# Kernel tuning notes

Hardware: AMD Instinct MI355X
Metric: run time of the kernel (lower is better)

Reference implementation:

```python
import jax, jax.numpy as jnp
import numpy as np


def setup_inputs() -> dict:
    key = jax.random.key(0)
    k1, k2 = jax.random.split(key)
    B, Te, Td, D = 8, 2048, 2048, 256
    encoder_outputs = jax.random.normal(k1, (B, Te, D), dtype=jnp.float32)
    decoder_outputs = jax.random.normal(k2, (B, Td, D), dtype=jnp.float32)
    return {"encoder_outputs": encoder_outputs, "decoder_outputs": decoder_outputs}


def reference(encoder_outputs, decoder_outputs):
    # score[b, e, t] = enc[b, e, :] . dec[b, t, :]   -> [B, Te, Td]
    score = jnp.einsum('bed,btd->bet', encoder_outputs, decoder_outputs)
    # softmax over the encoder-time axis (axis=1), matching K.softmax(..., axis=1)
    attn = jax.nn.softmax(score, axis=1)
    # context[b, t, d] = sum_e attn[b, e, t] * enc[b, e, d]
    # (original does expand_dims + broadcast-mul + sum; einsum is the same math)
    context = jnp.einsum('bet,bed->btd', attn, encoder_outputs)
    return jnp.concatenate([decoder_outputs, context], axis=-1)  # [B, Td, 2D]
```

## Files before the change

### kernel.cpp

```cpp
#include <hip/hip_runtime.h>


#define B_   8
#define TE   2048
#define TD   2048
#define D_   256
#define NIT  32

typedef _Float16 f16x8 __attribute__((ext_vector_type(8)));
typedef float f32x4 __attribute__((ext_vector_type(4)));

__device__ __forceinline__ unsigned pk2(float a, float b) {
  unsigned short ua = __builtin_bit_cast(unsigned short, (_Float16)a);
  unsigned short ub = __builtin_bit_cast(unsigned short, (_Float16)b);
  return (unsigned)ua | ((unsigned)ub << 16);
}

#define GLOAD16(gsrc, ldst)                                                  \
  __builtin_amdgcn_global_load_lds(                                          \
      (const __attribute__((address_space(1))) unsigned int*)(const void*)(gsrc), \
      (__attribute__((address_space(3))) unsigned int*)(void*)(ldst), 16, 0, 0)

__global__ __launch_bounds__(256) void prep_fused(const float* __restrict__ enc,
                                                  _Float16* __restrict__ encK,
                                                  _Float16* __restrict__ encVt) {
  __shared__ float tile[64][65];
  int bid = blockIdx.x;
  int b = bid >> 7, r = bid & 127;
  int et = r >> 2, dt = r & 3;
  int e0 = et * 64, d0 = dt * 64;
  int tx = threadIdx.x & 63, ty = threadIdx.x >> 6;
  const float* src = enc + ((size_t)b * TE + e0) * D_ + d0;
#pragma unroll
  for (int i = 0; i < 16; ++i)
    tile[i * 4 + ty][tx] = src[(size_t)(i * 4 + ty) * D_ + tx];
  __syncthreads();

  _Float16* kout = encK + ((size_t)b * TE + e0) * D_ + d0;
#pragma unroll
  for (int i = 0; i < 2; ++i) {
    int ci = i * 256 + threadIdx.x;
    int e = ci >> 3, xl = ci & 7;
    int xs = xl ^ (e & 7);
    const float* s8 = &tile[e][xs * 8];
    f16x8 h;
#pragma unroll
    for (int j = 0; j < 8; ++j) h[j] = (_Float16)s8[j];
    *(f16x8*)(kout + (size_t)e * D_ + xl * 8) = h;
  }
#pragma unroll
  for (int i = 0; i < 2; ++i) {
    int u = i * 256 + threadIdx.x;
    int y = u & 3, d_loc = (u >> 2) & 63, ctl = u >> 8;
    int s = (d_loc >> 1) & 3;
    int ebase = ctl * 32 + ((y ^ s) << 3);
    f16x8 h;
#pragma unroll
    for (int j = 0; j < 8; ++j) h[j] = (_Float16)tile[ebase + j][d_loc];
    size_t o = (((size_t)b * 64 + et * 2 + ctl) * 256 + d0 + d_loc) * 32 + y * 8;
    *(f16x8*)(encVt + o) = h;
  }
}

__global__ __launch_bounds__(512, 2) void luong_main(
    const _Float16* __restrict__ encK,
    const _Float16* __restrict__ encVt,
    const float* __restrict__ dec,
    float* __restrict__ out) {
  extern __shared__ char lds[];
  const int tid = threadIdx.x;
  const int lane = tid & 63, wave = tid >> 6;
  const int wr = wave >> 2, wc = wave & 3;
  const int g = lane >> 4, c = lane & 15;

  int bidl = (blockIdx.x & 7) * 32 + (blockIdx.x >> 3);
  const int b = bidl >> 5;
  const int q0 = (bidl & 31) * 64;
  const int t = q0 + wc * 16 + c;

  const float* decB = dec + (size_t)b * TD * D_;
  float* outB = out + (size_t)b * TD * (2 * D_);

  f16x8 qh[8], ql[8];
  {
    const float* qrow = decB + (size_t)t * D_;
#pragma unroll
    for (int dc = 0; dc < 8; ++dc) {
      float4 v0 = *(const float4*)(qrow + dc * 32 + 8 * g);
      float4 v1 = *(const float4*)(qrow + dc * 32 + 8 * g + 4);
      float f[8] = {v0.x, v0.y, v0.z, v0.w, v1.x, v1.y, v1.z, v1.w};
      f16x8 H, L;
#pragma unroll
      for (int j = 0; j < 8; ++j) {
        _Float16 h = (_Float16)f[j];
        H[j] = h;
        L[j] = (_Float16)(f[j] - (float)h);
      }
      qh[dc] = H; ql[dc] = L;
    }
  }

  const _Float16* kbase = encK + ((size_t)b * TE + wr * 1024) * D_;
  const _Float16* vbase = encVt + ((size_t)b * 64 + wr * 32) * 8192;

  auto STAGE = [&](int buf, int it) {
    char* Kd = lds + (size_t)(buf * 2 + wr) * 32768;
    char* Vd = Kd + 16384;
    const _Float16* ks = kbase + (size_t)it * 8192;
    const _Float16* vs = vbase + (size_t)it * 8192;
#pragma unroll
    for (int q = 0; q < 4; ++q) {
      int chunk = wc * 256 + q * 64 + lane;
      GLOAD16(ks + (size_t)chunk * 8, Kd + wc * 4096 + q * 1024);
      GLOAD16(vs + (size_t)chunk * 8, Vd + wc * 4096 + q * 1024);
    }
  };

  float m_run = -INFINITY, l_run = 0.f;
  f32x4 ctx[16];
#pragma unroll
  for (int i = 0; i < 16; ++i) ctx[i] = (f32x4){0.f, 0.f, 0.f, 0.f};

  f32x4 sA, sB;
  f16x8 bfrag;

  auto QK = [&](const char* Kb, f32x4& oA, f32x4& oB) {
    oA = (f32x4){0.f, 0.f, 0.f, 0.f};
    oB = (f32x4){0.f, 0.f, 0.f, 0.f};
    const int el0 = c, el1 = 16 + c;
#pragma unroll
    for (int dc = 0; dc < 8; ++dc) {
      int x = dc * 4 + g;
      int xsw = (x & 24) | ((x ^ el0) & 7);
      f16x8 k0 = *(const f16x8*)(Kb + el0 * 512 + (xsw << 4));
      f16x8 k1 = *(const f16x8*)(Kb + el1 * 512 + (xsw << 4));
      oA = __builtin_amdgcn_mfma_f32_16x16x32_f16(k0, qh[dc], oA, 0, 0, 0);
      oA = __builtin_amdgcn_mfma_f32_16x16x32_f16(k0, ql[dc], oA, 0, 0, 0);
      oB = __builtin_amdgcn_mfma_f32_16x16x32_f16(k1, qh[dc], oB, 0, 0, 0);
      oB = __builtin_amdgcn_mfma_f32_16x16x32_f16(k1, ql[dc], oB, 0, 0, 0);
    }
  };

  auto PV = [&](const char* Vb) {
#pragma unroll
    for (int dt = 0; dt < 16; ++dt) {
      int row = dt * 16 + c;
      f16x8 af = *(const f16x8*)(Vb + row * 64 + ((g ^ ((row >> 1) & 3)) << 4));
      ctx[dt] = __builtin_amdgcn_mfma_f32_16x16x32_f16(af, bfrag, ctx[dt], 0, 0, 0);
    }
  };

  auto SOFTMAX = [&]() {
    float vmax = fmaxf(fmaxf(fmaxf(sA[0], sA[1]), fmaxf(sA[2], sA[3])),
                       fmaxf(fmaxf(sB[0], sB[1]), fmaxf(sB[2], sB[3])));
    vmax = fmaxf(vmax, __shfl_xor(vmax, 16, 64));
    vmax = fmaxf(vmax, __shfl_xor(vmax, 32, 64));
    if (!__all(vmax <= m_run + 8.0f)) {
      float m_new = fmaxf(m_run, vmax);
      float alpha = __expf(m_run - m_new);
      l_run *= alpha;
#pragma unroll
      for (int i = 0; i < 16; ++i) ctx[i] *= alpha;
      m_run = m_new;
    }
    float p0 = __expf(sA[0] - m_run), p1 = __expf(sA[1] - m_run);
    float p2 = __expf(sA[2] - m_run), p3 = __expf(sA[3] - m_run);
    float p4 = __expf(sB[0] - m_run), p5 = __expf(sB[1] - m_run);
    float p6 = __expf(sB[2] - m_run), p7 = __expf(sB[3] - m_run);
    float ps = ((p0 + p1) + (p2 + p3)) + ((p4 + p5) + (p6 + p7));
    ps += __shfl_xor(ps, 16, 64);
    ps += __shfl_xor(ps, 32, 64);
    l_run += ps;
    unsigned w00 = pk2(p0, p1), w10 = pk2(p2, p3);
    unsigned w01 = pk2(p4, p5), w11 = pk2(p6, p7);
    int srcA = (2 * (g & 1)) * 16 + c, srcB = srcA + 16;
    int y0 = __shfl((int)w00, srcA, 64), y1 = __shfl((int)w10, srcA, 64);
    int y2 = __shfl((int)w00, srcB, 64), y3 = __shfl((int)w10, srcB, 64);
    int z0 = __shfl((int)w01, srcA, 64), z1 = __shfl((int)w11, srcA, 64);
    int z2 = __shfl((int)w01, srcB, 64), z3 = __shfl((int)w11, srcB, 64);
    int4 bi = (g >> 1) ? make_int4(z0, z1, z2, z3) : make_int4(y0, y1, y2, y3);
    bfrag = __builtin_bit_cast(f16x8, bi);
  };

  STAGE(0, 0);
#pragma unroll
  for (int i = 0; i < 8; ++i) {
    int ci = tid + 512 * i;
    int rr = ci >> 6, d4 = (ci & 63) << 2;
    *(float4*)(outB + (size_t)(q0 + rr) * 512 + d4) =
        *(const float4*)(decB + (size_t)(q0 + rr) * 256 + d4);
  }
  __syncthreads();
  STAGE(1, 1);
  QK(lds + (size_t)wr * 32768, sA, sB);
  SOFTMAX();
  __syncthreads();

#pragma unroll 2
  for (int it = 0; it < NIT; ++it) {
    const int cur = it & 1;
    const char* bufC = lds + (size_t)(cur * 2 + wr) * 32768;
    const char* bufN = lds + (size_t)((cur ^ 1) * 2 + wr) * 32768;
    f32x4 nA, nB;
    __builtin_amdgcn_s_setprio(1);
    if (it + 1 < NIT) QK(bufN, nA, nB);
    PV(bufC + 16384);
    __builtin_amdgcn_s_setprio(0);
    __syncthreads();
    if (it + 2 < NIT) STAGE(cur, it + 2);
    if (it + 1 < NIT) {
      sA = nA; sB = nB;
      SOFTMAX();
      __syncthreads();
    }
  }

  float* mlb = (float*)(lds + 69632);
  if (lane < 16) {
    mlb[((wr * 4 + wc) * 16 + c) * 2 + 0] = m_run;
    mlb[((wr * 4 + wc) * 16 + c) * 2 + 1] = l_run;
  }
  __syncthreads();
  float m_o = mlb[(((1 - wr) * 4 + wc) * 16 + c) * 2 + 0];
  float l_o = mlb[(((1 - wr) * 4 + wc) * 16 + c) * 2 + 1];
  float M = fmaxf(m_run, m_o);
  float fme = __expf(m_run - M);
  float L = l_run * fme + l_o * __expf(m_o - M);
  float invL = 1.0f / L;

  float* Xb = (float*)lds + wc * 4352;
  if (wr == 1) {
#pragma unroll
    for (int dt = 0; dt < 16; ++dt)
#pragma unroll
      for (int r = 0; r < 4; ++r) {
        int d = dt * 16 + 4 * g + r;
        Xb[d * 17 + c] = ctx[dt][r] * fme;
      }
  }
  __syncthreads();
  if (wr == 0) {
    float* orow = outB + (size_t)t * 512 + 256;
#pragma unroll
    for (int dt = 0; dt < 16; ++dt) {
      float4 v;
      float vv[4];
#pragma unroll
      for (int r = 0; r < 4; ++r) {
        int d = dt * 16 + 4 * g + r;
        vv[r] = (ctx[dt][r] * fme + Xb[d * 17 + c]) * invL;
      }
      v.x = vv[0]; v.y = vv[1]; v.z = vv[2]; v.w = vv[3];
      *(float4*)(orow + dt * 16 + 4 * g) = v;
    }
  }
}

extern "C" void kernel_launch(void* const* d_in, const int* in_sizes, int n_in,
                              void* d_out, int out_size, void* d_ws, size_t ws_size,
                              hipStream_t stream) {
  const float* enc = (const float*)d_in[0];
  const float* dec = (const float*)d_in[1];
  float* out = (float*)d_out;
  (void)in_sizes; (void)n_in; (void)out_size; (void)ws_size;

  _Float16* encK  = (_Float16*)d_ws;
  _Float16* encVt = (_Float16*)((char*)d_ws + 8388608);

  prep_fused<<<1024, 256, 0, stream>>>(enc, encK, encVt);
  luong_main<<<256, 512, 131072, stream>>>(encK, encVt, dec, out);
}
```

Baseline: 165.4 us.

## Restructure main loop to prefetch two stages and use explicit vmcnt waits

```diff
diff --git a/kernel.cpp b/kernel.cpp
--- a/kernel.cpp
+++ b/kernel.cpp
@@ -81,6 +81,33 @@
   const float* decB = dec + (size_t)b * TD * D_;
   float* outB = out + (size_t)b * TD * (2 * D_);
 
+  const _Float16* kbase = encK + ((size_t)b * TE + wr * 1024) * D_;
+  const _Float16* vbase = encVt + ((size_t)b * 64 + wr * 32) * 8192;
+
+  auto STAGE = [&](int buf, int it) {
+    char* Kd = lds + (size_t)(buf * 2 + wr) * 32768;
+    char* Vd = Kd + 16384;
+    const _Float16* ks = kbase + (size_t)it * 8192;
+    const _Float16* vs = vbase + (size_t)it * 8192;
+#pragma unroll
+    for (int q = 0; q < 4; ++q) {
+      int chunk = wc * 256 + q * 64 + lane;
+      GLOAD16(ks + (size_t)chunk * 8, Kd + wc * 4096 + q * 1024);
+      GLOAD16(vs + (size_t)chunk * 8, Vd + wc * 4096 + q * 1024);
+    }
+  };
+
+  STAGE(0, 0);
+  STAGE(1, 1);
+
+#pragma unroll
+  for (int i = 0; i < 8; ++i) {
+    int ci = tid + 512 * i;
+    int rr = ci >> 6, d4 = (ci & 63) << 2;
+    *(float4*)(outB + (size_t)(q0 + rr) * 512 + d4) =
+        *(const float4*)(decB + (size_t)(q0 + rr) * 256 + d4);
+  }
+
   f16x8 qh[8], ql[8];
   {
     const float* qrow = decB + (size_t)t * D_;
@@ -100,22 +127,6 @@
     }
   }
 
-  const _Float16* kbase = encK + ((size_t)b * TE + wr * 1024) * D_;
-  const _Float16* vbase = encVt + ((size_t)b * 64 + wr * 32) * 8192;
-
-  auto STAGE = [&](int buf, int it) {
-    char* Kd = lds + (size_t)(buf * 2 + wr) * 32768;
-    char* Vd = Kd + 16384;
-    const _Float16* ks = kbase + (size_t)it * 8192;
-    const _Float16* vs = vbase + (size_t)it * 8192;
-#pragma unroll
-    for (int q = 0; q < 4; ++q) {
-      int chunk = wc * 256 + q * 64 + lane;
-      GLOAD16(ks + (size_t)chunk * 8, Kd + wc * 4096 + q * 1024);
-      GLOAD16(vs + (size_t)chunk * 8, Vd + wc * 4096 + q * 1024);
-    }
-  };
-
   float m_run = -INFINITY, l_run = 0.f;
   f32x4 ctx[16];
 #pragma unroll
@@ -124,9 +135,9 @@
   f32x4 sA, sB;
   f16x8 bfrag;
 
-  auto QK = [&](const char* Kb, f32x4& oA, f32x4& oB) {
-    oA = (f32x4){0.f, 0.f, 0.f, 0.f};
-    oB = (f32x4){0.f, 0.f, 0.f, 0.f};
+  auto QK = [&](const char* Kb) {
+    sA = (f32x4){0.f, 0.f, 0.f, 0.f};
+    sB = (f32x4){0.f, 0.f, 0.f, 0.f};
     const int el0 = c, el1 = 16 + c;
 #pragma unroll
     for (int dc = 0; dc < 8; ++dc) {
@@ -134,10 +145,10 @@
       int xsw = (x & 24) | ((x ^ el0) & 7);
       f16x8 k0 = *(const f16x8*)(Kb + el0 * 512 + (xsw << 4));
       f16x8 k1 = *(const f16x8*)(Kb + el1 * 512 + (xsw << 4));
-      oA = __builtin_amdgcn_mfma_f32_16x16x32_f16(k0, qh[dc], oA, 0, 0, 0);
-      oA = __builtin_amdgcn_mfma_f32_16x16x32_f16(k0, ql[dc], oA, 0, 0, 0);
-      oB = __builtin_amdgcn_mfma_f32_16x16x32_f16(k1, qh[dc], oB, 0, 0, 0);
-      oB = __builtin_amdgcn_mfma_f32_16x16x32_f16(k1, ql[dc], oB, 0, 0, 0);
+      sA = __builtin_amdgcn_mfma_f32_16x16x32_f16(k0, qh[dc], sA, 0, 0, 0);
+      sA = __builtin_amdgcn_mfma_f32_16x16x32_f16(k0, ql[dc], sA, 0, 0, 0);
+      sB = __builtin_amdgcn_mfma_f32_16x16x32_f16(k1, qh[dc], sB, 0, 0, 0);
+      sB = __builtin_amdgcn_mfma_f32_16x16x32_f16(k1, ql[dc], sB, 0, 0, 0);
     }
   };
 
@@ -182,40 +193,41 @@
     bfrag = __builtin_bit_cast(f16x8, bi);
   };
 
-  STAGE(0, 0);
-#pragma unroll
-  for (int i = 0; i < 8; ++i) {
-    int ci = tid + 512 * i;
-    int rr = ci >> 6, d4 = (ci & 63) << 2;
-    *(float4*)(outB + (size_t)(q0 + rr) * 512 + d4) =
-        *(const float4*)(decB + (size_t)(q0 + rr) * 256 + d4);
-  }
-  __syncthreads();
-  STAGE(1, 1);
-  QK(lds + (size_t)wr * 32768, sA, sB);
-  SOFTMAX();
-  __syncthreads();
+  asm volatile("s_waitcnt vmcnt(8)" ::: "memory");
+  __builtin_amdgcn_sched_barrier(0);
+  __builtin_amdgcn_s_barrier();
+  __builtin_amdgcn_sched_barrier(0);
 
 #pragma unroll 2
   for (int it = 0; it < NIT; ++it) {
     const int cur = it & 1;
     const char* bufC = lds + (size_t)(cur * 2 + wr) * 32768;
-    const char* bufN = lds + (size_t)((cur ^ 1) * 2 + wr) * 32768;
-    f32x4 nA, nB;
+
     __builtin_amdgcn_s_setprio(1);
-    if (it + 1 < NIT) QK(bufN, nA, nB);
+    QK(bufC);
+    __builtin_amdgcn_s_setprio(0);
+    SOFTMAX();
+    __builtin_amdgcn_s_setprio(1);
     PV(bufC + 16384);
     __builtin_amdgcn_s_setprio(0);
-    __syncthreads();
-    if (it + 2 < NIT) STAGE(cur, it + 2);
-    if (it + 1 < NIT) {
-      sA = nA; sB = nB;
-      SOFTMAX();
-      __syncthreads();
-    }
-  }
-
-  float* mlb = (float*)(lds + 69632);
+
+    asm volatile("s_waitcnt lgkmcnt(0)" ::: "memory");
+    __builtin_amdgcn_sched_barrier(0);
+    __builtin_amdgcn_s_barrier();
+    __builtin_amdgcn_sched_barrier(0);
+
+    if (it + 2 < NIT) {
+      STAGE(cur, it + 2);
+      asm volatile("s_waitcnt vmcnt(8)" ::: "memory");
+    } else {
+      asm volatile("s_waitcnt vmcnt(0)" ::: "memory");
+    }
+    __builtin_amdgcn_sched_barrier(0);
+    __builtin_amdgcn_s_barrier();
+    __builtin_amdgcn_sched_barrier(0);
+  }
+
+  float* mlb = (float*)(lds + 130048);
   if (lane < 16) {
     mlb[((wr * 4 + wc) * 16 + c) * 2 + 0] = m_run;
     mlb[((wr * 4 + wc) * 16 + c) * 2 + 1] = l_run;
```

After: 157.3 us. -4.9%, faster.

## Load V fragments directly from global, stage only K in LDS, drop P shuffles

Applied to the files above, without the earlier changes.

```diff
diff --git a/kernel.cpp b/kernel.cpp
--- a/kernel.cpp
+++ b/kernel.cpp
@@ -8,13 +8,8 @@
 #define NIT  32
 
 typedef _Float16 f16x8 __attribute__((ext_vector_type(8)));
+typedef _Float16 f16x4 __attribute__((ext_vector_type(4)));
 typedef float f32x4 __attribute__((ext_vector_type(4)));
-
-__device__ __forceinline__ unsigned pk2(float a, float b) {
-  unsigned short ua = __builtin_bit_cast(unsigned short, (_Float16)a);
-  unsigned short ub = __builtin_bit_cast(unsigned short, (_Float16)b);
-  return (unsigned)ua | ((unsigned)ub << 16);
-}
 
 #define GLOAD16(gsrc, ldst)                                                  \
   __builtin_amdgcn_global_load_lds(                                          \
@@ -51,13 +46,14 @@
 #pragma unroll
   for (int i = 0; i < 2; ++i) {
     int u = i * 256 + threadIdx.x;
-    int y = u & 3, d_loc = (u >> 2) & 63, ctl = u >> 8;
-    int s = (d_loc >> 1) & 3;
-    int ebase = ctl * 32 + ((y ^ s) << 3);
+    int gpos = u & 3, d_loc = (u >> 2) & 63, ctl = u >> 8;
+    int eb = ctl * 32 + 4 * gpos;
     f16x8 h;
 #pragma unroll
-    for (int j = 0; j < 8; ++j) h[j] = (_Float16)tile[ebase + j][d_loc];
-    size_t o = (((size_t)b * 64 + et * 2 + ctl) * 256 + d0 + d_loc) * 32 + y * 8;
+    for (int j = 0; j < 4; ++j) h[j] = (_Float16)tile[eb + j][d_loc];
+#pragma unroll
+    for (int j = 0; j < 4; ++j) h[4 + j] = (_Float16)tile[eb + 16 + j][d_loc];
+    size_t o = (((size_t)b * 64 + et * 2 + ctl) * 256 + d0 + d_loc) * 32 + gpos * 8;
     *(f16x8*)(encVt + o) = h;
   }
 }
@@ -70,20 +66,43 @@
   extern __shared__ char lds[];
   const int tid = threadIdx.x;
   const int lane = tid & 63, wave = tid >> 6;
-  const int wr = wave >> 2, wc = wave & 3;
+  const int wr = wave >> 2, tw = wave & 3;
   const int g = lane >> 4, c = lane & 15;
 
   int bidl = (blockIdx.x & 7) * 32 + (blockIdx.x >> 3);
   const int b = bidl >> 5;
   const int q0 = (bidl & 31) * 64;
-  const int t = q0 + wc * 16 + c;
+  const int tbase = q0 + tw * 16;
 
   const float* decB = dec + (size_t)b * TD * D_;
   float* outB = out + (size_t)b * TD * (2 * D_);
 
+  const _Float16* kbase = encK + ((size_t)b * TE + wr * 1024) * D_;
+  const _Float16* vbase = encVt + ((size_t)b * 64 + wr * 32) * 8192;
+
+  char* grpK = lds + (size_t)wr * 32768;
+
+  auto KSTAGE = [&](int slot, int it) {
+    char* Kd = grpK + slot * 16384 + tw * 4096;
+    const _Float16* ks = kbase + (size_t)it * 8192 + tw * 2048;
+#pragma unroll
+    for (int q = 0; q < 4; ++q)
+      GLOAD16(ks + q * 512 + lane * 8, Kd + q * 1024 + lane * 16);
+  };
+
+  KSTAGE(0, 0); KSTAGE(1, 1);
+
+#pragma unroll
+  for (int i = 0; i < 8; ++i) {
+    int ci = tid + 512 * i;
+    int rr = ci >> 6, d4 = (ci & 63) << 2;
+    *(float4*)(outB + (size_t)(q0 + rr) * 512 + d4) =
+        *(const float4*)(decB + (size_t)(q0 + rr) * 256 + d4);
+  }
+
   f16x8 qh[8], ql[8];
   {
-    const float* qrow = decB + (size_t)t * D_;
+    const float* qrow = decB + (size_t)(tbase + c) * D_;
 #pragma unroll
     for (int dc = 0; dc < 8; ++dc) {
       float4 v0 = *(const float4*)(qrow + dc * 32 + 8 * g);
@@ -100,157 +119,114 @@
     }
   }
 
-  const _Float16* kbase = encK + ((size_t)b * TE + wr * 1024) * D_;
-  const _Float16* vbase = encVt + ((size_t)b * 64 + wr * 32) * 8192;
-
-  auto STAGE = [&](int buf, int it) {
-    char* Kd = lds + (size_t)(buf * 2 + wr) * 32768;
-    char* Vd = Kd + 16384;
-    const _Float16* ks = kbase + (size_t)it * 8192;
-    const _Float16* vs = vbase + (size_t)it * 8192;
-#pragma unroll
-    for (int q = 0; q < 4; ++q) {
-      int chunk = wc * 256 + q * 64 + lane;
-      GLOAD16(ks + (size_t)chunk * 8, Kd + wc * 4096 + q * 1024);
-      GLOAD16(vs + (size_t)chunk * 8, Vd + wc * 4096 + q * 1024);
-    }
-  };
+  __syncthreads();
 
   float m_run = -INFINITY, l_run = 0.f;
   f32x4 ctx[16];
 #pragma unroll
   for (int i = 0; i < 16; ++i) ctx[i] = (f32x4){0.f, 0.f, 0.f, 0.f};
 
-  f32x4 sA, sB;
-  f16x8 bfrag;
-
-  auto QK = [&](const char* Kb, f32x4& oA, f32x4& oB) {
-    oA = (f32x4){0.f, 0.f, 0.f, 0.f};
-    oB = (f32x4){0.f, 0.f, 0.f, 0.f};
-    const int el0 = c, el1 = 16 + c;
+  for (int it = 0; it < NIT; ++it) {
+    const int slot = it & 1;
+    const char* Kb = grpK + slot * 16384;
+
+    f16x8 vreg[16];
+    const _Float16* vt = vbase + (size_t)it * 8192;
+#pragma unroll
+    for (int dt = 0; dt < 16; ++dt)
+      vreg[dt] = *(const f16x8*)(vt + (dt * 16 + c) * 32 + g * 8);
+
+    f32x4 sA = (f32x4){0.f, 0.f, 0.f, 0.f};
+    f32x4 sB = (f32x4){0.f, 0.f, 0.f, 0.f};
 #pragma unroll
     for (int dc = 0; dc < 8; ++dc) {
       int x = dc * 4 + g;
-      int xsw = (x & 24) | ((x ^ el0) & 7);
-      f16x8 k0 = *(const f16x8*)(Kb + el0 * 512 + (xsw << 4));
-      f16x8 k1 = *(const f16x8*)(Kb + el1 * 512 + (xsw << 4));
-      oA = __builtin_amdgcn_mfma_f32_16x16x32_f16(k0, qh[dc], oA, 0, 0, 0);
-      oA = __builtin_amdgcn_mfma_f32_16x16x32_f16(k0, ql[dc], oA, 0, 0, 0);
-      oB = __builtin_amdgcn_mfma_f32_16x16x32_f16(k1, qh[dc], oB, 0, 0, 0);
-      oB = __builtin_amdgcn_mfma_f32_16x16x32_f16(k1, ql[dc], oB, 0, 0, 0);
-    }
-  };
-
-  auto PV = [&](const char* Vb) {
+      int xsw = (x & 24) | ((x ^ c) & 7);
+      f16x8 k0 = *(const f16x8*)(Kb + c * 512 + (xsw << 4));
+      f16x8 k1 = *(const f16x8*)(Kb + (16 + c) * 512 + (xsw << 4));
+      sA = __builtin_amdgcn_mfma_f32_16x16x32_f16(k0, qh[dc], sA, 0, 0, 0);
+      sA = __builtin_amdgcn_mfma_f32_16x16x32_f16(k0, ql[dc], sA, 0, 0, 0);
+      sB = __builtin_amdgcn_mfma_f32_16x16x32_f16(k1, qh[dc], sB, 0, 0, 0);
+      sB = __builtin_amdgcn_mfma_f32_16x16x32_f16(k1, ql[dc], sB, 0, 0, 0);
+    }
+
+    f16x4 bfA, bfB;
+    {
+      float vmax = fmaxf(fmaxf(fmaxf(sA[0], sA[1]), fmaxf(sA[2], sA[3])),
+                         fmaxf(fmaxf(sB[0], sB[1]), fmaxf(sB[2], sB[3])));
+      vmax = fmaxf(vmax, __shfl_xor(vmax, 16, 64));
+      vmax = fmaxf(vmax, __shfl_xor(vmax, 32, 64));
+      if (!__all(vmax <= m_run + 8.0f)) {
+        float mn = fmaxf(m_run, vmax);
+        float alpha = __expf(m_run - mn);
+        l_run *= alpha;
+#pragma unroll
+        for (int i = 0; i < 16; ++i) ctx[i] *= alpha;
+        m_run = mn;
+      }
+      float p0 = __expf(sA[0] - m_run), p1 = __expf(sA[1] - m_run);
+      float p2 = __expf(sA[2] - m_run), p3 = __expf(sA[3] - m_run);
+      float p4 = __expf(sB[0] - m_run), p5 = __expf(sB[1] - m_run);
+      float p6 = __expf(sB[2] - m_run), p7 = __expf(sB[3] - m_run);
+      float ps = ((p0 + p1) + (p2 + p3)) + ((p4 + p5) + (p6 + p7));
+      ps += __shfl_xor(ps, 16, 64);
+      ps += __shfl_xor(ps, 32, 64);
+      l_run += ps;
+      bfA[0] = (_Float16)p0; bfA[1] = (_Float16)p1;
+      bfA[2] = (_Float16)p2; bfA[3] = (_Float16)p3;
+      bfB[0] = (_Float16)p4; bfB[1] = (_Float16)p5;
+      bfB[2] = (_Float16)p6; bfB[3] = (_Float16)p7;
+    }
+
 #pragma unroll
     for (int dt = 0; dt < 16; ++dt) {
-      int row = dt * 16 + c;
-      f16x8 af = *(const f16x8*)(Vb + row * 64 + ((g ^ ((row >> 1) & 3)) << 4));
-      ctx[dt] = __builtin_amdgcn_mfma_f32_16x16x32_f16(af, bfrag, ctx[dt], 0, 0, 0);
-    }
-  };
-
-  auto SOFTMAX = [&]() {
-    float vmax = fmaxf(fmaxf(fmaxf(sA[0], sA[1]), fmaxf(sA[2], sA[3])),
-                       fmaxf(fmaxf(sB[0], sB[1]), fmaxf(sB[2], sB[3])));
-    vmax = fmaxf(vmax, __shfl_xor(vmax, 16, 64));
-    vmax = fmaxf(vmax, __shfl_xor(vmax, 32, 64));
-    if (!__all(vmax <= m_run + 8.0f)) {
-      float m_new = fmaxf(m_run, vmax);
-      float alpha = __expf(m_run - m_new);
-      l_run *= alpha;
-#pragma unroll
-      for (int i = 0; i < 16; ++i) ctx[i] *= alpha;
-      m_run = m_new;
-    }
-    float p0 = __expf(sA[0] - m_run), p1 = __expf(sA[1] - m_run);
-    float p2 = __expf(sA[2] - m_run), p3 = __expf(sA[3] - m_run);
-    float p4 = __expf(sB[0] - m_run), p5 = __expf(sB[1] - m_run);
-    float p6 = __expf(sB[2] - m_run), p7 = __expf(sB[3] - m_run);
-    float ps = ((p0 + p1) + (p2 + p3)) + ((p4 + p5) + (p6 + p7));
-    ps += __shfl_xor(ps, 16, 64);
-    ps += __shfl_xor(ps, 32, 64);
-    l_run += ps;
-    unsigned w00 = pk2(p0, p1), w10 = pk2(p2, p3);
-    unsigned w01 = pk2(p4, p5), w11 = pk2(p6, p7);
-    int srcA = (2 * (g & 1)) * 16 + c, srcB = srcA + 16;
-    int y0 = __shfl((int)w00, srcA, 64), y1 = __shfl((int)w10, srcA, 64);
-    int y2 = __shfl((int)w00, srcB, 64), y3 = __shfl((int)w10, srcB, 64);
-    int z0 = __shfl((int)w01, srcA, 64), z1 = __shfl((int)w11, srcA, 64);
-    int z2 = __shfl((int)w01, srcB, 64), z3 = __shfl((int)w11, srcB, 64);
-    int4 bi = (g >> 1) ? make_int4(z0, z1, z2, z3) : make_int4(y0, y1, y2, y3);
-    bfrag = __builtin_bit_cast(f16x8, bi);
-  };
-
-  STAGE(0, 0);
-#pragma unroll
-  for (int i = 0; i < 8; ++i) {
-    int ci = tid + 512 * i;
-    int rr = ci >> 6, d4 = (ci & 63) << 2;
-    *(float4*)(outB + (size_t)(q0 + rr) * 512 + d4) =
-        *(const float4*)(decB + (size_t)(q0 + rr) * 256 + d4);
-  }
-  __syncthreads();
-  STAGE(1, 1);
-  QK(lds + (size_t)wr * 32768, sA, sB);
-  SOFTMAX();
-  __syncthreads();
-
-#pragma unroll 2
-  for (int it = 0; it < NIT; ++it) {
-    const int cur = it & 1;
-    const char* bufC = lds + (size_t)(cur * 2 + wr) * 32768;
-    const char* bufN = lds + (size_t)((cur ^ 1) * 2 + wr) * 32768;
-    f32x4 nA, nB;
-    __builtin_amdgcn_s_setprio(1);
-    if (it + 1 < NIT) QK(bufN, nA, nB);
-    PV(bufC + 16384);
-    __builtin_amdgcn_s_setprio(0);
+      int4 vi = __builtin_bit_cast(int4, vreg[dt]);
+      f16x4 a0 = __builtin_bit_cast(f16x4, make_int2(vi.x, vi.y));
+      f16x4 a1 = __builtin_bit_cast(f16x4, make_int2(vi.z, vi.w));
+      ctx[dt] = __builtin_amdgcn_mfma_f32_16x16x16f16(a0, bfA, ctx[dt], 0, 0, 0);
+      ctx[dt] = __builtin_amdgcn_mfma_f32_16x16x16f16(a1, bfB, ctx[dt], 0, 0, 0);
+    }
+
     __syncthreads();
-    if (it + 2 < NIT) STAGE(cur, it + 2);
-    if (it + 1 < NIT) {
-      sA = nA; sB = nB;
-      SOFTMAX();
-      __syncthreads();
-    }
-  }
-
-  float* mlb = (float*)(lds + 69632);
-  if (lane < 16) {
-    mlb[((wr * 4 + wc) * 16 + c) * 2 + 0] = m_run;
-    mlb[((wr * 4 + wc) * 16 + c) * 2 + 1] = l_run;
-  }
-  __syncthreads();
-  float m_o = mlb[(((1 - wr) * 4 + wc) * 16 + c) * 2 + 0];
-  float l_o = mlb[(((1 - wr) * 4 + wc) * 16 + c) * 2 + 1];
-  float M = fmaxf(m_run, m_o);
+    if (it + 2 < NIT) KSTAGE(slot, it + 2);
+  }
+
+  float* mlb = (float*)(lds + 66560);
+  if (g == 0) {
+    mlb[(wave * 16 + c) * 2 + 0] = m_run;
+    mlb[(wave * 16 + c) * 2 + 1] = l_run;
+  }
+  __syncthreads();
+  int partner = (1 - wr) * 4 + tw;
+  float mo = mlb[(partner * 16 + c) * 2 + 0];
+  float lo = mlb[(partner * 16 + c) * 2 + 1];
+  float M = fmaxf(m_run, mo);
   float fme = __expf(m_run - M);
-  float L = l_run * fme + l_o * __expf(m_o - M);
+  float L = l_run * fme + lo * __expf(mo - M);
   float invL = 1.0f / L;
 
-  float* Xb = (float*)lds + wc * 4352;
+  float* Xb = (float*)lds;
   if (wr == 1) {
 #pragma unroll
     for (int dt = 0; dt < 16; ++dt)
 #pragma unroll
       for (int r = 0; r < 4; ++r) {
         int d = dt * 16 + 4 * g + r;
-        Xb[d * 17 + c] = ctx[dt][r] * fme;
+        Xb[d * 65 + tw * 16 + c] = ctx[dt][r] * fme;
       }
   }
   __syncthreads();
   if (wr == 0) {
-    float* orow = outB + (size_t)t * 512 + 256;
+    float* orow = outB + (size_t)(tbase + c) * 512 + 256;
 #pragma unroll
     for (int dt = 0; dt < 16; ++dt) {
-      float4 v;
       float vv[4];
 #pragma unroll
       for (int r = 0; r < 4; ++r) {
         int d = dt * 16 + 4 * g + r;
-        vv[r] = (ctx[dt][r] * fme + Xb[d * 17 + c]) * invL;
-      }
-      v.x = vv[0]; v.y = vv[1]; v.z = vv[2]; v.w = vv[3];
+        vv[r] = (ctx[dt][r] * fme + Xb[d * 65 + tw * 16 + c]) * invL;
+      }
+      float4 v; v.x = vv[0]; v.y = vv[1]; v.z = vv[2]; v.w = vv[3];
       *(float4*)(orow + dt * 16 + 4 * g) = v;
     }
   }
@@ -268,5 +244,5 @@
   _Float16* encVt = (_Float16*)((char*)d_ws + 8388608);
 
   prep_fused<<<1024, 256, 0, stream>>>(enc, encK, encVt);
-  luong_main<<<256, 512, 131072, stream>>>(encK, encVt, dec, out);
+  luong_main<<<256, 512, 67584, stream>>>(encK, encVt, dec, out);
 }
```

After: 178.5 us. 1.08x slower.
